# Performance work log

Hardware: AMD Instinct MI355X
Metric: run time of the kernel (lower is better)

## Reference

```python
import jax, jax.numpy as jnp
import numpy as np

B, S, H = 2, 2048, 2048
E, K, HID = 8, 2, 4096          # num_experts, top-k, expert hidden (2*H)
NH, HD = 8, 256                  # attention heads, head_dim
MS, MD = 256, 512                # memory_size, memory_dim
RSTEPS, RD = 3, 512              # reasoning steps, reasoning_dim
SCALE = 16.0                     # sqrt(head_dim)


def setup_inputs() -> dict:
    key = jax.random.key(0)
    ks = iter(jax.random.split(key, 64))
    def w(shape, s=0.02):
        return (jax.random.normal(next(ks), shape, jnp.float32) * s)
    z = lambda *shape: jnp.zeros(shape, jnp.float32)
    inp = {
        'hidden_states': jax.random.normal(next(ks), (B, S, H), jnp.float32),
        'attention_mask': jnp.zeros((B, S), jnp.float32),  # 0 = unmasked (faithful: mask*-1e9 added)
        # MoE
        'gate_w': w((H, E)), 'gate_b': z(E),
        'moe_w1': w((E, H, HID)), 'moe_b1': z(E, HID),
        'moe_w2': w((E, HID, H)), 'moe_b2': z(E, H),
        # memory-augmented attention
        'q_w': w((H, H)), 'q_b': z(H),
        'k_w': w((H, H)), 'k_b': z(H),
        'v_w': w((H, H)), 'v_b': z(H),
        'o_w': w((H, H)), 'o_b': z(H),
        'mem_values': jax.random.normal(next(ks), (MS, MD), jnp.float32),
        'mem_proj_w': w((MD, H)), 'mem_proj_b': z(H),
        'mem_attn_w': w((H, MS)), 'mem_attn_b': z(MS),
        # hierarchical reasoning (stacked over steps)
        'rs_w1': w((RSTEPS, H, RD)), 'rs_b1': z(RSTEPS, RD),
        'rs_w2': w((RSTEPS, RD, H)), 'rs_b2': z(RSTEPS, H),
        'ln_g': jnp.ones((RSTEPS, H), jnp.float32), 'ln_b': z(RSTEPS, H),
        'hg_w1': w((RSTEPS, H, H // 4)), 'hg_b1': z(RSTEPS, H // 4),
        'hg_w2': w((RSTEPS, H // 4, 1)), 'hg_b2': z(RSTEPS, 1),
        'integ_w': w((RSTEPS * H, H)), 'integ_b': z(H),
    }
    return inp


def _layernorm(x, g, b, eps=1e-5):
    m = x.mean(-1, keepdims=True)
    v = ((x - m) ** 2).mean(-1, keepdims=True)
    return (x - m) / jnp.sqrt(v + eps) * g + b


def _forward(hidden_states, attention_mask, gate_w, gate_b, moe_w1, moe_b1, moe_w2, moe_b2,
             q_w, q_b, k_w, k_b, v_w, v_b, o_w, o_b, mem_values, mem_proj_w, mem_proj_b,
             mem_attn_w, mem_attn_b, rs_w1, rs_b1, rs_w2, rs_b2, ln_g, ln_b,
             hg_w1, hg_b1, hg_w2, hg_b2, integ_w, integ_b):
    h = hidden_states
    N = B * S
    # ---- Mixture of Experts (top-k routing, dense combine-weight formulation) ----
    x_flat = h.reshape(N, H)
    gate_probs = jax.nn.softmax(x_flat @ gate_w + gate_b, axis=-1)        # [N,E]
    topk_s, topk_i = jax.lax.top_k(gate_probs, K)                          # [N,K]
    topk_p = jax.nn.softmax(topk_s, axis=-1)                               # renormalize over top-k
    comb = jnp.zeros((N, E), x_flat.dtype).at[jnp.arange(N)[:, None], topk_i].add(topk_p)
    h1 = jax.nn.relu(jnp.einsum('nd,edh->neh', x_flat, moe_w1) + moe_b1)   # [N,E,HID]
    eo = jnp.einsum('neh,ehd->ned', h1, moe_w2) + moe_b2                   # [N,E,H]
    moe_out = jnp.einsum('ned,ne->nd', eo, comb).reshape(B, S, H)
    h = h + 0.5 * moe_out
    # ---- Memory-augmented attention ----
    q = (h @ q_w + q_b).reshape(B, S, NH, HD).transpose(0, 2, 1, 3)
    k = (h @ k_w + k_b).reshape(B, S, NH, HD).transpose(0, 2, 1, 3)
    v = (h @ v_w + v_b).reshape(B, S, NH, HD).transpose(0, 2, 1, 3)
    scores = jnp.einsum('bhqd,bhkd->bhqk', q, k) / SCALE
    scores = scores + attention_mask[:, None, None, :] * (-1e9)
    probs = jax.nn.softmax(scores, axis=-1)
    attn = jnp.einsum('bhqk,bhkd->bhqd', probs, v).transpose(0, 2, 1, 3).reshape(B, S, H)
    mem_p = jax.nn.softmax(h @ mem_attn_w + mem_attn_b, axis=-1)           # [B,S,MS]
    mem_o = (mem_p @ mem_values) @ mem_proj_w + mem_proj_b                 # [B,S,H]
    mem_out = (attn + 0.3 * mem_o) @ o_w + o_b
    h = h + mem_out
    # ---- Hierarchical reasoning ----
    cur = h
    outs = []
    for i in range(RSTEPS):
        so = jax.nn.relu(cur @ rs_w1[i] + rs_b1[i]) @ rs_w2[i] + rs_b2[i]
        so = _layernorm(so, ln_g[i], ln_b[i])
        g = jax.nn.sigmoid(jax.nn.relu(cur @ hg_w1[i] + hg_b1[i]) @ hg_w2[i] + hg_b2[i])  # [B,S,1]
        cur = cur + g * so
        outs.append(cur)
    final = jnp.concatenate(outs, axis=-1) @ integ_w + integ_b
    return h + final


def reference(hidden_states, attention_mask, gate_w, gate_b, moe_w1, moe_b1, moe_w2, moe_b2,
              q_w, q_b, k_w, k_b, v_w, v_b, o_w, o_b, mem_values, mem_proj_w, mem_proj_b,
              mem_attn_w, mem_attn_b, rs_w1, rs_b1, rs_w2, rs_b2, ln_g, ln_b,
              hg_w1, hg_b1, hg_w2, hg_b2, integ_w, integ_b):
    return _forward(hidden_states, attention_mask, gate_w, gate_b, moe_w1, moe_b1, moe_w2, moe_b2,
                    q_w, q_b, k_w, k_b, v_w, v_b, o_w, o_b, mem_values, mem_proj_w, mem_proj_b,
                    mem_attn_w, mem_attn_b, rs_w1, rs_b1, rs_w2, rs_b2, ln_g, ln_b,
                    hg_w1, hg_b1, hg_w2, hg_b2, integ_w, integ_b)
```

## Files before the change

kernel.cpp:

```cpp
#include <hip/hip_runtime.h>
#include <string.h>


typedef __attribute__((ext_vector_type(4))) float f32x4;
typedef __attribute__((ext_vector_type(8))) __bf16 bf16x8;

#define NTOK 4096
#define HDIM 2048
#define AS1 __attribute__((address_space(1)))
#define AS3 __attribute__((address_space(3)))

__device__ __forceinline__ unsigned short f2bf(float f) {
  unsigned u = __float_as_uint(f);
  unsigned r = (u + 0x7fffu + ((u >> 16) & 1u)) >> 16;
  return (unsigned short)r;
}
__device__ __forceinline__ float bf2f(unsigned short u) {
  return __uint_as_float(((unsigned)u) << 16);
}
__device__ __forceinline__ void unpack8(uint4 r, float* v) {
  v[0]=bf2f((unsigned short)(r.x&0xffff)); v[1]=bf2f((unsigned short)(r.x>>16));
  v[2]=bf2f((unsigned short)(r.y&0xffff)); v[3]=bf2f((unsigned short)(r.y>>16));
  v[4]=bf2f((unsigned short)(r.z&0xffff)); v[5]=bf2f((unsigned short)(r.z>>16));
  v[6]=bf2f((unsigned short)(r.w&0xffff)); v[7]=bf2f((unsigned short)(r.w>>16));
}
__device__ __forceinline__ uint4 pack8(const float* v) {
  uint4 r;
  r.x = (unsigned)f2bf(v[0]) | ((unsigned)f2bf(v[1])<<16);
  r.y = (unsigned)f2bf(v[2]) | ((unsigned)f2bf(v[3])<<16);
  r.z = (unsigned)f2bf(v[4]) | ((unsigned)f2bf(v[5])<<16);
  r.w = (unsigned)f2bf(v[6]) | ((unsigned)f2bf(v[7])<<16);
  return r;
}

__global__ void k_tconv(const float* __restrict__ in, unsigned short* __restrict__ out,
                        int R, int C, long inB, long outB) {
  __shared__ float tl[32][33];
  const int z = blockIdx.z;
  const float* ip = in + (long)z * inB;
  unsigned short* op = out + (long)z * outB;
  const int tx = threadIdx.x & 31, ty = threadIdx.x >> 5;
  const int c0 = blockIdx.x * 32, r0 = blockIdx.y * 32;
#pragma unroll
  for (int i = 0; i < 4; i++)
    tl[ty + i*8][tx] = ip[(long)(r0 + ty + i*8) * C + c0 + tx];
  __syncthreads();
#pragma unroll
  for (int i = 0; i < 4; i++)
    op[(long)(c0 + ty + i*8) * R + r0 + tx] = f2bf(tl[tx][ty + i*8]);
}

__global__ void k_cvt(const float* __restrict__ in, unsigned short* __restrict__ out, long n4) {
  long i = (long)blockIdx.x * blockDim.x + threadIdx.x;
  if (i < n4) {
    float4 v = ((const float4*)in)[i];
    float vv[4] = {v.x, v.y, v.z, v.w};
    union { unsigned short u[4]; uint2 d; } p;
#pragma unroll
    for (int j = 0; j < 4; j++) p.u[j] = f2bf(vv[j]);
    ((uint2*)out)[i] = p.d;
  }
}

__global__ void k_tvact(const unsigned short* __restrict__ qkv, unsigned short* __restrict__ vT) {
  __shared__ unsigned short tl[32][33];
  const int z = blockIdx.z, b = z >> 3, hh = z & 7;
  const unsigned short* ip = qkv + (long)b * 2048 * 6144 + 4096 + hh * 256;
  unsigned short* op = vT + (long)z * 256 * 2048;
  const int tx = threadIdx.x & 31, ty = threadIdx.x >> 5;
  const int d0 = blockIdx.x * 32, s0 = blockIdx.y * 32;
#pragma unroll
  for (int i = 0; i < 4; i++)
    tl[ty + i*8][tx] = ip[(long)(s0 + ty + i*8) * 6144 + d0 + tx];
  __syncthreads();
#pragma unroll
  for (int i = 0; i < 4; i++)
    op[(long)(d0 + ty + i*8) * 2048 + s0 + tx] = tl[tx][ty + i*8];
}

__global__ void k_maskvec(const float* __restrict__ m, float* __restrict__ mv) {
  int i = blockIdx.x * 256 + threadIdx.x;
  if (i < 4096) mv[i] = -1e9f * m[i];
}

__global__ void k_zero(int* p) { if (threadIdx.x < 8) p[threadIdx.x] = 0; }

__global__ void k_cat3(const float* __restrict__ a, const float* __restrict__ b,
                       const float* __restrict__ c, float* __restrict__ o) {
  int i = blockIdx.x * 256 + threadIdx.x;
  if (i < 2048) { o[i] = a[i]; o[2048 + i] = b[i]; o[4096 + i] = c[i]; }
}

__global__ void k_cat2x3(const float* __restrict__ a, const float* __restrict__ b,
                         float* __restrict__ o) {
  int i = blockIdx.x * 256 + threadIdx.x;
  if (i < 1536) { int s = i >> 9, c = i & 511; o[s * 1024 + c] = a[i]; o[s * 1024 + 512 + c] = b[i]; }
}

__global__ void k_gate(const float* __restrict__ x, const float* __restrict__ gw,
                       const float* __restrict__ gb, int* __restrict__ meta,
                       int* __restrict__ e0a, int* __restrict__ e1a,
                       float* __restrict__ w0a, float* __restrict__ w1a) {
  const int wv = threadIdx.x >> 6, ln = threadIdx.x & 63;
  const int n = blockIdx.x * 4 + wv;
  const float* xr = x + (long)n * HDIM;
  float s[8] = {0,0,0,0,0,0,0,0};
  for (int k = ln; k < HDIM; k += 64) {
    float xv = xr[k];
    const float* g = gw + (long)k * 8;
#pragma unroll
    for (int e = 0; e < 8; e++) s[e] += xv * g[e];
  }
#pragma unroll
  for (int e = 0; e < 8; e++)
    for (int d = 32; d; d >>= 1) s[e] += __shfl_xor(s[e], d);
  if (ln == 0) {
    float mx = -1e30f;
#pragma unroll
    for (int e = 0; e < 8; e++) { s[e] += gb[e]; mx = fmaxf(mx, s[e]); }
    float p[8], sum = 0.f;
#pragma unroll
    for (int e = 0; e < 8; e++) { p[e] = expf(s[e] - mx); sum += p[e]; }
    float inv = 1.f / sum;
#pragma unroll
    for (int e = 0; e < 8; e++) p[e] *= inv;
    int e0 = 0;
    for (int e = 1; e < 8; e++) if (p[e] > p[e0]) e0 = e;
    int e1 = (e0 == 0) ? 1 : 0;
    for (int e = 0; e < 8; e++) if (e != e0 && p[e] > p[e1]) e1 = e;
    float q = expf(p[e1] - p[e0]);
    float w0 = 1.f / (1.f + q), w1 = q / (1.f + q);
    e0a[n] = e0; e1a[n] = e1; w0a[n] = w0; w1a[n] = w1;
    atomicAdd(&meta[e0], 1); atomicAdd(&meta[e1], 1);
  }
}

__global__ void k_buildmap(int* meta) {
  if (threadIdx.x == 0 && blockIdx.x == 0) {
    int cum = 0, nT = 0;
    for (int e = 0; e < 8; e++) {
      int c = meta[e];
      meta[16 + e] = cum; meta[24 + e] = cum + c; meta[8 + e] = 0;
      int t = (c + 127) >> 7;
      for (int i = 0; i < t; i++) { meta[33 + nT] = e; meta[129 + nT] = cum + i * 128; nT++; }
      cum += c;
    }
    meta[32] = nT;
  }
}

__global__ void k_scatter(int* __restrict__ meta, const int* __restrict__ e0a,
                          const int* __restrict__ e1a, int* __restrict__ s0a,
                          int* __restrict__ s1a, int* __restrict__ srcTok) {
  const int n = blockIdx.x * 256 + threadIdx.x;
  if (n < NTOK) {
    int e0 = e0a[n], e1 = e1a[n];
    int s0 = meta[16 + e0] + atomicAdd(&meta[8 + e0], 1);
    int s1 = meta[16 + e1] + atomicAdd(&meta[8 + e1], 1);
    s0a[n] = s0; s1a[n] = s1; srcTok[s0] = n; srcTok[s1] = n;
  }
}

__global__ void k_gather(const unsigned short* __restrict__ xb, const int* __restrict__ srcTok,
                         unsigned short* __restrict__ xg) {
  const int r = blockIdx.x;
  int n = srcTok[r]; if (n < 0 || n >= NTOK) n = 0;
  ((uint4*)(xg + (long)r * HDIM))[threadIdx.x] =
      ((const uint4*)(xb + (long)n * HDIM))[threadIdx.x];
}

__global__ void k_combine(const float* __restrict__ h, const unsigned short* __restrict__ eo,
                          const int* __restrict__ s0a, const int* __restrict__ s1a,
                          const float* __restrict__ w0a, const float* __restrict__ w1a,
                          float* __restrict__ h2, unsigned short* __restrict__ h2b) {
  const int n = blockIdx.x, c = threadIdx.x * 8;
  const float w0 = w0a[n], w1 = w1a[n];
  uint4 a = *(const uint4*)(eo + (long)s0a[n] * HDIM + c);
  uint4 b = *(const uint4*)(eo + (long)s1a[n] * HDIM + c);
  float va[8], vb[8]; unpack8(a, va); unpack8(b, vb);
  const float* hr = h + (long)n * HDIM + c;
  float o[8];
#pragma unroll
  for (int j = 0; j < 8; j++) o[j] = hr[j] + 0.5f * (w0 * va[j] + w1 * vb[j]);
  float* h2r = h2 + (long)n * HDIM + c;
#pragma unroll
  for (int j = 0; j < 8; j++) h2r[j] = o[j];
  *(uint4*)(h2b + (long)n * HDIM + c) = pack8(o);
}

__global__ void k_softmax2048(unsigned short* __restrict__ p) {
  const long r = blockIdx.x;
  unsigned short* row = p + r * 2048;
  const int t = threadIdx.x, wv = t >> 6, ln = t & 63;
  uint4 raw = ((const uint4*)row)[t];
  float v[8]; unpack8(raw, v);
  float m = v[0];
#pragma unroll
  for (int j = 1; j < 8; j++) m = fmaxf(m, v[j]);
  for (int d = 32; d; d >>= 1) m = fmaxf(m, __shfl_xor(m, d));
  __shared__ float sm[4], ssum[4];
  if (ln == 0) sm[wv] = m;
  __syncthreads();
  m = fmaxf(fmaxf(sm[0], sm[1]), fmaxf(sm[2], sm[3]));
  float s = 0.f;
#pragma unroll
  for (int j = 0; j < 8; j++) { v[j] = expf(v[j] - m); s += v[j]; }
  for (int d = 32; d; d >>= 1) s += __shfl_xor(s, d);
  if (ln == 0) ssum[wv] = s;
  __syncthreads();
  s = ssum[0] + ssum[1] + ssum[2] + ssum[3];
  const float inv = 1.f / s;
#pragma unroll
  for (int j = 0; j < 8; j++) v[j] *= inv;
  ((uint4*)row)[t] = pack8(v);
}

__global__ void k_softmax256(const float* __restrict__ in, unsigned short* __restrict__ out) {
  const int wv = threadIdx.x >> 6, ln = threadIdx.x & 63;
  const long r = (long)blockIdx.x * 4 + wv;
  const float4 v4 = ((const float4*)(in + r * 256))[ln];
  float v[4] = {v4.x, v4.y, v4.z, v4.w};
  float m = fmaxf(fmaxf(v[0], v[1]), fmaxf(v[2], v[3]));
  for (int d = 32; d; d >>= 1) m = fmaxf(m, __shfl_xor(m, d));
  float s = 0.f;
#pragma unroll
  for (int j = 0; j < 4; j++) { v[j] = expf(v[j] - m); s += v[j]; }
  for (int d = 32; d; d >>= 1) s += __shfl_xor(s, d);
  const float inv = 1.f / s;
  union { unsigned short u[4]; uint2 d2; } p;
#pragma unroll
  for (int j = 0; j < 4; j++) p.u[j] = f2bf(v[j] * inv);
  ((uint2*)(out + r * 256))[ln] = p.d2;
}

__global__ void k_gdot(const unsigned short* __restrict__ g1, long ld, const float* __restrict__ w,
                       const float* __restrict__ bb, float* __restrict__ gv) {
  const int wv = threadIdx.x >> 6, ln = threadIdx.x & 63;
  const int n = blockIdx.x * 4 + wv;
  uint4 raw = *(const uint4*)(g1 + (long)n * ld + ln * 8);
  float v[8]; unpack8(raw, v);
  const float4 wa = ((const float4*)w)[ln * 2];
  const float4 wb = ((const float4*)w)[ln * 2 + 1];
  float s = v[0]*wa.x + v[1]*wa.y + v[2]*wa.z + v[3]*wa.w
          + v[4]*wb.x + v[5]*wb.y + v[6]*wb.z + v[7]*wb.w;
  for (int d = 32; d; d >>= 1) s += __shfl_xor(s, d);
  if (ln == 0) gv[n] = 1.f / (1.f + expf(-(s + bb[0])));
}

__global__ void k_lnupdate(const float* __restrict__ so, const float* __restrict__ curIn,
                           const float* __restrict__ gv, const float* __restrict__ lng,
                           const float* __restrict__ lnb, float* __restrict__ curOut,
                           unsigned short* __restrict__ curbOut, unsigned short* __restrict__ outs,
                           int step) {
  const int n = blockIdx.x, t = threadIdx.x, wv = t >> 6, ln = t & 63, c = t * 8;
  const float* row = so + (long)n * 2048 + c;
  float x[8];
#pragma unroll
  for (int j = 0; j < 8; j++) x[j] = row[j];
  float s1 = 0.f, s2 = 0.f;
#pragma unroll
  for (int j = 0; j < 8; j++) { s1 += x[j]; s2 += x[j] * x[j]; }
  for (int d = 32; d; d >>= 1) { s1 += __shfl_xor(s1, d); s2 += __shfl_xor(s2, d); }
  __shared__ float a1[4], a2[4];
  if (ln == 0) { a1[wv] = s1; a2[wv] = s2; }
  __syncthreads();
  s1 = a1[0] + a1[1] + a1[2] + a1[3];
  s2 = a2[0] + a2[1] + a2[2] + a2[3];
  const float mean = s1 * (1.f / 2048.f);
  const float var = s2 * (1.f / 2048.f) - mean * mean;
  const float rstd = rsqrtf(var + 1e-5f);
  const float g = gv[n];
  const float* ci = curIn + (long)n * 2048 + c;
  float o[8];
#pragma unroll
  for (int j = 0; j < 8; j++) {
    float l = (x[j] - mean) * rstd * lng[c + j] + lnb[c + j];
    o[j] = ci[j] + g * l;
  }
  float* co = curOut + (long)n * 2048 + c;
#pragma unroll
  for (int j = 0; j < 8; j++) co[j] = o[j];
  *(uint4*)(curbOut + (long)n * 2048 + c) = pack8(o);
  *(uint4*)(outs + (long)n * 6144 + (long)step * 2048 + c) = pack8(o);
}

struct GArgs {
  const unsigned short* A; long lda, aSO, aSI;
  const unsigned short* Bt; long ldb, bSO, bSI;
  int M, N, K;
  const float* adv; long advSO, advSI;
  float alpha, rscale;
  const float* rF; long ldrF, rfSO, rfSI;
  const unsigned short* rB; long ldrB, rbSO, rbSI;
  float* oF; long ldoF, ofSO, ofSI;
  unsigned short* oB; long ldoB, obSO, obSI;
  const int* meta;
};

template <int MOE, int RELU, int RESID, int OUTF, int OUTB>
__global__ __launch_bounds__(512) void gemm_bt(GArgs g) {
  __shared__ unsigned short lds[2 * 16384];
  const int t = threadIdx.x, wv = t >> 6, ln = t & 63, ln15 = ln & 15;
  const int lr8 = ln >> 3;
  const int lsl = (ln & 7) ^ lr8;
  const int bz = blockIdx.z;
  int row0, rowMax;
  const unsigned short *A, *Bt;
  long advO = 0, rFO = 0, rBO = 0, oFO = 0, oBO = 0;
  if constexpr (MOE) {
    const int ty = blockIdx.y;
    if (ty >= g.meta[32]) return;
    const int e = g.meta[33 + ty];
    row0 = g.meta[129 + ty]; rowMax = g.meta[24 + e];
    A = g.A; Bt = g.Bt + (long)e * g.bSO;
    advO = (long)e * g.advSO;
  } else {
    row0 = blockIdx.y << 7; rowMax = g.M;
    const long bo = (long)(bz >> 3), bi = (long)(bz & 7);
    A = g.A + bo * g.aSO + bi * g.aSI;
    Bt = g.Bt + bo * g.bSO + bi * g.bSI;
    advO = bo * g.advSO + bi * g.advSI;
    rFO = bo * g.rfSO + bi * g.rfSI;
    rBO = bo * g.rbSO + bi * g.rbSI;
    oFO = bo * g.ofSO + bi * g.ofSI;
    oBO = bo * g.obSO + bi * g.obSI;
  }
  const int col0 = blockIdx.x << 7;
  const long lda = g.lda, ldb = g.ldb;
  const int wm = (wv >> 2) << 6;
  const int wc = (wv & 3) << 5;

  auto STAGE = [&](int kt, unsigned base) {
    const long kk = ((long)kt << 6) + (lsl << 3);
#pragma unroll
    for (int l = 0; l < 2; ++l) {
      const int rb = (wv << 4) + (l << 3);
      int gr = row0 + rb + lr8;
      if constexpr (MOE) gr = (gr < rowMax) ? gr : (rowMax - 1);
      __builtin_amdgcn_global_load_lds(
          (const AS1 void*)(A + (long)gr * lda + kk),
          (AS3 void*)(lds + base + (rb << 6)), 16, 0, 0);
    }
#pragma unroll
    for (int l = 0; l < 2; ++l) {
      const int rb = (wv << 4) + (l << 3);
      __builtin_amdgcn_global_load_lds(
          (const AS1 void*)(Bt + (long)(col0 + rb + lr8) * ldb + kk),
          (AS3 void*)(lds + base + 8192 + (rb << 6)), 16, 0, 0);
    }
  };

  const f32x4 fz = {0.f, 0.f, 0.f, 0.f};
  f32x4 acc[4][2];
#pragma unroll
  for (int i = 0; i < 4; i++)
#pragma unroll
    for (int j = 0; j < 2; j++) acc[i][j] = fz;

  const int nt = g.K >> 6;

  STAGE(0, 0);
  asm volatile("s_waitcnt vmcnt(0)" ::: "memory");
  __builtin_amdgcn_s_barrier();

  for (int kt = 0; kt < nt; ++kt) {
    const unsigned aB = (kt & 1) ? 16384u : 0u;
    const unsigned nB = aB ^ 16384u;
    bf16x8 af[2][4], bg[2][2];
#pragma unroll
    for (int ks = 0; ks < 2; ++ks) {
      const int kb = (ks << 2) + (ln >> 4);
#pragma unroll
      for (int i = 0; i < 4; ++i) {
        const int r = wm + (i << 4) + ln15;
        af[ks][i] = *(const bf16x8*)(lds + aB + (r << 6) + ((kb ^ (r & 7)) << 3));
      }
#pragma unroll
      for (int j = 0; j < 2; ++j) {
        const int r = wc + (j << 4) + ln15;
        bg[ks][j] = *(const bf16x8*)(lds + aB + 8192 + (r << 6) + ((kb ^ (r & 7)) << 3));
      }
    }
    __builtin_amdgcn_sched_barrier(0);
    if (kt + 1 < nt) STAGE(kt + 1, nB);
    __builtin_amdgcn_sched_barrier(0);
    __builtin_amdgcn_s_setprio(1);
#pragma unroll
    for (int ks = 0; ks < 2; ++ks)
#pragma unroll
      for (int i = 0; i < 4; ++i)
#pragma unroll
        for (int j = 0; j < 2; ++j)
          acc[i][j] = __builtin_amdgcn_mfma_f32_16x16x32_bf16(af[ks][i], bg[ks][j], acc[i][j], 0, 0, 0);
    __builtin_amdgcn_s_setprio(0);
    asm volatile("s_waitcnt vmcnt(0)" ::: "memory");
    __builtin_amdgcn_s_barrier();
  }

#pragma unroll
  for (int i = 0; i < 4; i++) {
#pragma unroll
    for (int j = 0; j < 2; j++) {
      const int cc = col0 + wc + (j << 4) + ln15;
      const float av = g.adv ? g.adv[advO + cc] : 0.f;
#pragma unroll
      for (int r = 0; r < 4; r++) {
        const int rr = row0 + wm + (i << 4) + ((ln >> 4) << 2) + r;
        if (rr < rowMax) {
          float v = g.alpha * acc[i][j][r] + av;
          if constexpr (RELU) v = fmaxf(v, 0.f);
          if constexpr (RESID == 1) v = g.rF[rFO + (long)rr * g.ldrF + cc] + g.rscale * v;
          if constexpr (RESID == 2) v = bf2f(g.rB[rBO + (long)rr * g.ldrB + cc]) + g.rscale * v;
          if constexpr (OUTF) g.oF[oFO + (long)rr * g.ldoF + cc] = v;
          if constexpr (OUTB) g.oB[oBO + (long)rr * g.ldoB + cc] = f2bf(v);
        }
      }
    }
  }
}

static constexpr size_t O_W1T = 0;
static constexpr size_t O_W2T = O_W1T + (size_t)8 * 4096 * 2048 * 2;
static constexpr size_t O_QT  = O_W2T + (size_t)8 * 4096 * 2048 * 2;
static constexpr size_t O_KT  = O_QT + (size_t)2048 * 2048 * 2;
static constexpr size_t O_VWT = O_KT + (size_t)2048 * 2048 * 2;
static constexpr size_t O_OT  = O_VWT + (size_t)2048 * 2048 * 2;
static constexpr size_t O_MAT = O_OT + (size_t)2048 * 2048 * 2;
static constexpr size_t O_MPT = O_MAT + (size_t)256 * 2048 * 2;
static constexpr size_t O_MVT = O_MPT + (size_t)2048 * 512 * 2;
static constexpr size_t O_RH1 = O_MVT + (size_t)512 * 256 * 2;
static constexpr size_t O_RS2 = O_RH1 + (size_t)3 * 1024 * 2048 * 2;
static constexpr size_t O_IGT = O_RS2 + (size_t)3 * 2048 * 512 * 2;
static constexpr size_t O_META= O_IGT + (size_t)2048 * 6144 * 2;
static constexpr size_t O_E0  = O_META + 4096;
static constexpr size_t O_E1  = O_E0 + 16384;
static constexpr size_t O_W0  = O_E1 + 16384;
static constexpr size_t O_W1  = O_W0 + 16384;
static constexpr size_t O_S0  = O_W1 + 16384;
static constexpr size_t O_S1  = O_S0 + 16384;
static constexpr size_t O_SRC = O_S1 + 16384;
static constexpr size_t O_MSK = O_SRC + 32768;
static constexpr size_t O_GV  = O_MSK + 16384;
static constexpr size_t O_QKVB= O_GV + 16384;
static constexpr size_t O_RHB = O_QKVB + 6144 * 4;
static constexpr size_t O_H2  = O_RHB + 3072 * 4;
static constexpr size_t O_H2B = O_H2 + (size_t)4096 * 2048 * 4;
static constexpr size_t O_H3  = O_H2B + (size_t)4096 * 2048 * 2;
static constexpr size_t O_H3B = O_H3 + (size_t)4096 * 2048 * 4;
static constexpr size_t O_ATT = O_H3B + (size_t)4096 * 2048 * 2;
static constexpr size_t O_AO2 = O_ATT + (size_t)4096 * 2048 * 2;
static constexpr size_t O_MLG = O_AO2 + (size_t)4096 * 2048 * 2;
static constexpr size_t O_MPB = O_MLG + (size_t)4096 * 256 * 4;
static constexpr size_t O_MPV = O_MPB + (size_t)4096 * 256 * 2;
static constexpr size_t O_AR  = O_MPV + (size_t)4096 * 512 * 2;
static constexpr size_t O_XB = O_AR;
static constexpr size_t O_XG = O_XB + (size_t)4096 * 2048 * 2;
static constexpr size_t O_H1 = O_XG + (size_t)8192 * 2048 * 2;
static constexpr size_t O_EO = O_H1 + (size_t)8192 * 4096 * 2;
static constexpr size_t O_QB = O_AR;
static constexpr size_t O_VT = O_QB + (size_t)3 * 4096 * 2048 * 2;
static constexpr size_t O_SC = O_VT + (size_t)4096 * 2048 * 2;
static constexpr size_t O_T1 = O_AR;
static constexpr size_t O_SOB= O_T1 + (size_t)4096 * 1024 * 2;
static constexpr size_t O_CUR= O_SOB + (size_t)4096 * 2048 * 4;
static constexpr size_t O_CRB= O_CUR + (size_t)4096 * 2048 * 4;
static constexpr size_t O_OUS= O_CRB + (size_t)4096 * 2048 * 2;

extern "C" void kernel_launch(void* const* d_in, const int* in_sizes, int n_in,
                              void* d_out, int out_size, void* d_ws, size_t ws_size,
                              hipStream_t stream) {
  (void)in_sizes; (void)n_in; (void)out_size; (void)ws_size;
  const float* h        = (const float*)d_in[0];
  const float* mask     = (const float*)d_in[1];
  const float* gate_w   = (const float*)d_in[2];
  const float* gate_b   = (const float*)d_in[3];
  const float* moe_w1   = (const float*)d_in[4];
  const float* moe_b1   = (const float*)d_in[5];
  const float* moe_w2   = (const float*)d_in[6];
  const float* moe_b2   = (const float*)d_in[7];
  const float* q_w      = (const float*)d_in[8];
  const float* q_b      = (const float*)d_in[9];
  const float* k_w      = (const float*)d_in[10];
  const float* k_b      = (const float*)d_in[11];
  const float* v_w      = (const float*)d_in[12];
  const float* v_b      = (const float*)d_in[13];
  const float* o_w      = (const float*)d_in[14];
  const float* o_b      = (const float*)d_in[15];
  const float* mem_vals = (const float*)d_in[16];
  const float* mproj_w  = (const float*)d_in[17];
  const float* mproj_b  = (const float*)d_in[18];
  const float* mattn_w  = (const float*)d_in[19];
  const float* mattn_b  = (const float*)d_in[20];
  const float* rs_w1    = (const float*)d_in[21];
  const float* rs_b1    = (const float*)d_in[22];
  const float* rs_w2    = (const float*)d_in[23];
  const float* rs_b2    = (const float*)d_in[24];
  const float* ln_g     = (const float*)d_in[25];
  const float* ln_b     = (const float*)d_in[26];
  const float* hg_w1    = (const float*)d_in[27];
  const float* hg_b1    = (const float*)d_in[28];
  const float* hg_w2    = (const float*)d_in[29];
  const float* hg_b2    = (const float*)d_in[30];
  const float* integ_w  = (const float*)d_in[31];
  const float* integ_b  = (const float*)d_in[32];

  char* ws = (char*)d_ws;
  auto U = [&](size_t o) { return (unsigned short*)(ws + o); };
  auto F = [&](size_t o) { return (float*)(ws + o); };
  auto I = [&](size_t o) { return (int*)(ws + o); };

  k_tconv<<<dim3(128, 64, 8), 256, 0, stream>>>(moe_w1, U(O_W1T), 2048, 4096, 8388608, 8388608);
  k_tconv<<<dim3(64, 128, 8), 256, 0, stream>>>(moe_w2, U(O_W2T), 4096, 2048, 8388608, 8388608);
  k_tconv<<<dim3(64, 64, 1), 256, 0, stream>>>(q_w, U(O_QT), 2048, 2048, 0, 0);
  k_tconv<<<dim3(64, 64, 1), 256, 0, stream>>>(k_w, U(O_KT), 2048, 2048, 0, 0);
  k_tconv<<<dim3(64, 64, 1), 256, 0, stream>>>(v_w, U(O_VWT), 2048, 2048, 0, 0);
  k_tconv<<<dim3(64, 64, 1), 256, 0, stream>>>(o_w, U(O_OT), 2048, 2048, 0, 0);
  k_tconv<<<dim3(8, 64, 1), 256, 0, stream>>>(mattn_w, U(O_MAT), 2048, 256, 0, 0);
  k_tconv<<<dim3(64, 16, 1), 256, 0, stream>>>(mproj_w, U(O_MPT), 512, 2048, 0, 0);
  k_tconv<<<dim3(16, 8, 1), 256, 0, stream>>>(mem_vals, U(O_MVT), 256, 512, 0, 0);
  k_tconv<<<dim3(16, 64, 3), 256, 0, stream>>>(rs_w1, U(O_RH1), 2048, 512, 2048 * 512, 1024 * 2048);
  k_tconv<<<dim3(16, 64, 3), 256, 0, stream>>>(hg_w1, U(O_RH1) + (size_t)512 * 2048, 2048, 512,
                                               2048 * 512, 1024 * 2048);
  k_tconv<<<dim3(64, 16, 3), 256, 0, stream>>>(rs_w2, U(O_RS2), 512, 2048, 512 * 2048, 512 * 2048);
  k_tconv<<<dim3(64, 192, 1), 256, 0, stream>>>(integ_w, U(O_IGT), 6144, 2048, 0, 0);
  k_cvt<<<8192, 256, 0, stream>>>(h, U(O_XB), 2097152);
  k_maskvec<<<16, 256, 0, stream>>>(mask, F(O_MSK));
  k_cat3<<<8, 256, 0, stream>>>(q_b, k_b, v_b, F(O_QKVB));
  k_cat2x3<<<6, 256, 0, stream>>>(rs_b1, hg_b1, F(O_RHB));
  k_zero<<<1, 64, 0, stream>>>(I(O_META));

  k_gate<<<1024, 256, 0, stream>>>(h, gate_w, gate_b, I(O_META), I(O_E0), I(O_E1), F(O_W0), F(O_W1));
  k_buildmap<<<1, 1, 0, stream>>>(I(O_META));
  k_scatter<<<16, 256, 0, stream>>>(I(O_META), I(O_E0), I(O_E1), I(O_S0), I(O_S1), I(O_SRC));
  k_gather<<<8192, 256, 0, stream>>>(U(O_XB), I(O_SRC), U(O_XG));

  GArgs z0; memset(&z0, 0, sizeof(z0)); z0.alpha = 1.f; z0.rscale = 1.f;
  {
    GArgs g = z0;
    g.A = U(O_XG); g.lda = 2048;
    g.Bt = U(O_W1T); g.ldb = 2048; g.bSO = (long)4096 * 2048;
    g.N = 4096; g.K = 2048;
    g.adv = moe_b1; g.advSO = 4096;
    g.oB = U(O_H1); g.ldoB = 4096;
    g.meta = I(O_META);
    gemm_bt<1, 1, 0, 0, 1><<<dim3(32, 72, 1), 512, 0, stream>>>(g);
  }
  {
    GArgs g = z0;
    g.A = U(O_H1); g.lda = 4096;
    g.Bt = U(O_W2T); g.ldb = 4096; g.bSO = (long)2048 * 4096;
    g.N = 2048; g.K = 4096;
    g.adv = moe_b2; g.advSO = 2048;
    g.oB = U(O_EO); g.ldoB = 2048;
    g.meta = I(O_META);
    gemm_bt<1, 0, 0, 0, 1><<<dim3(16, 72, 1), 512, 0, stream>>>(g);
  }
  k_combine<<<4096, 256, 0, stream>>>(h, U(O_EO), I(O_S0), I(O_S1), F(O_W0), F(O_W1),
                                      F(O_H2), U(O_H2B));

  {
    GArgs g = z0;
    g.A = U(O_H2B); g.lda = 2048; g.M = 4096; g.N = 6144; g.K = 2048;
    g.Bt = U(O_QT); g.ldb = 2048;
    g.adv = F(O_QKVB);
    g.oB = U(O_QB); g.ldoB = 6144;
    gemm_bt<0, 0, 0, 0, 1><<<dim3(48, 32, 1), 512, 0, stream>>>(g);
  }
  k_tvact<<<dim3(8, 64, 16), 256, 0, stream>>>(U(O_QB), U(O_VT));
  {
    GArgs g = z0;
    g.A = U(O_QB); g.lda = 6144; g.aSO = 12582912; g.aSI = 256;
    g.Bt = U(O_QB) + 2048; g.ldb = 6144; g.bSO = 12582912; g.bSI = 256;
    g.M = 2048; g.N = 2048; g.K = 256;
    g.adv = F(O_MSK); g.advSO = 2048; g.advSI = 0;
    g.alpha = 0.0625f;
    g.oB = U(O_SC); g.ldoB = 2048; g.obSO = 33554432; g.obSI = 4194304;
    gemm_bt<0, 0, 0, 0, 1><<<dim3(16, 16, 16), 512, 0, stream>>>(g);
  }
  k_softmax2048<<<32768, 256, 0, stream>>>(U(O_SC));
  {
    GArgs g = z0;
    g.A = U(O_SC); g.lda = 2048; g.aSO = 33554432; g.aSI = 4194304;
    g.Bt = U(O_VT); g.ldb = 2048; g.bSO = 4194304; g.bSI = 524288;
    g.M = 2048; g.N = 256; g.K = 2048;
    g.oB = U(O_ATT); g.ldoB = 2048; g.obSO = 4194304; g.obSI = 256;
    gemm_bt<0, 0, 0, 0, 1><<<dim3(2, 16, 16), 512, 0, stream>>>(g);
  }
  {
    GArgs g = z0;
    g.A = U(O_H2B); g.lda = 2048; g.Bt = U(O_MAT); g.ldb = 2048;
    g.M = 4096; g.N = 256; g.K = 2048;
    g.adv = mattn_b;
    g.oF = F(O_MLG); g.ldoF = 256;
    gemm_bt<0, 0, 0, 1, 0><<<dim3(2, 32, 1), 512, 0, stream>>>(g);
  }
  k_softmax256<<<1024, 256, 0, stream>>>(F(O_MLG), U(O_MPB));
  {
    GArgs g = z0;
    g.A = U(O_MPB); g.lda = 256; g.Bt = U(O_MVT); g.ldb = 256;
    g.M = 4096; g.N = 512; g.K = 256;
    g.oB = U(O_MPV); g.ldoB = 512;
    gemm_bt<0, 0, 0, 0, 1><<<dim3(4, 32, 1), 512, 0, stream>>>(g);
  }
  {
    GArgs g = z0;
    g.A = U(O_MPV); g.lda = 512; g.Bt = U(O_MPT); g.ldb = 512;
    g.M = 4096; g.N = 2048; g.K = 512;
    g.adv = mproj_b;
    g.rB = U(O_ATT); g.ldrB = 2048; g.rscale = 0.3f;
    g.oB = U(O_AO2); g.ldoB = 2048;
    gemm_bt<0, 0, 2, 0, 1><<<dim3(16, 32, 1), 512, 0, stream>>>(g);
  }
  {
    GArgs g = z0;
    g.A = U(O_AO2); g.lda = 2048; g.Bt = U(O_OT); g.ldb = 2048;
    g.M = 4096; g.N = 2048; g.K = 2048;
    g.adv = o_b;
    g.rF = F(O_H2); g.ldrF = 2048; g.rscale = 1.f;
    g.oF = F(O_H3); g.ldoF = 2048;
    g.oB = U(O_H3B); g.ldoB = 2048;
    gemm_bt<0, 0, 1, 1, 1><<<dim3(16, 32, 1), 512, 0, stream>>>(g);
  }

  for (int i = 0; i < 3; i++) {
    const unsigned short* curb = (i == 0) ? U(O_H3B) : U(O_CRB);
    const float* curf = (i == 0) ? F(O_H3) : F(O_CUR);
    {
      GArgs g = z0;
      g.A = curb; g.lda = 2048;
      g.Bt = U(O_RH1) + (size_t)i * 1024 * 2048; g.ldb = 2048;
      g.M = 4096; g.N = 1024; g.K = 2048;
      g.adv = F(O_RHB) + i * 1024;
      g.oB = U(O_T1); g.ldoB = 1024;
      gemm_bt<0, 1, 0, 0, 1><<<dim3(8, 32, 1), 512, 0, stream>>>(g);
    }
    {
      GArgs g = z0;
      g.A = U(O_T1); g.lda = 1024;
      g.Bt = U(O_RS2) + (size_t)i * 2048 * 512; g.ldb = 512;
      g.M = 4096; g.N = 2048; g.K = 512;
      g.adv = rs_b2 + i * 2048;
      g.oF = F(O_SOB); g.ldoF = 2048;
      gemm_bt<0, 0, 0, 1, 0><<<dim3(16, 32, 1), 512, 0, stream>>>(g);
    }
    k_gdot<<<1024, 256, 0, stream>>>(U(O_T1) + 512, 1024, hg_w2 + i * 512, hg_b2 + i, F(O_GV));
    k_lnupdate<<<4096, 256, 0, stream>>>(F(O_SOB), curf, F(O_GV), ln_g + i * 2048,
                                         ln_b + i * 2048, F(O_CUR), U(O_CRB), U(O_OUS), i);
  }
  {
    GArgs g = z0;
    g.A = U(O_OUS); g.lda = 6144; g.Bt = U(O_IGT); g.ldb = 6144;
    g.M = 4096; g.N = 2048; g.K = 6144;
    g.adv = integ_b;
    g.rF = F(O_H3); g.ldrF = 2048; g.rscale = 1.f;
    g.oF = (float*)d_out; g.ldoF = 2048;
    gemm_bt<0, 0, 1, 1, 0><<<dim3(16, 32, 1), 512, 0, stream>>>(g);
  }
}
```

Measured before the change: 1.738 ms.

## Add 256x256-tile GEMM kernel for MoE, QKV and score GEMMs

Adds a gemm256 kernel with 256x256 output tiles (each wave computes 128x64) and double-buffered 64 KB LDS, and uses it for the two MoE expert GEMMs, the QKV projection and the attention-score GEMM. MoE tile mapping in buildmap switches to 256-row groups to match. Larger tiles raise arithmetic intensity and reuse per LDS load. The loop now interleaves the A-fragment LDS reads with the MFMAs instead of loading all fragments up front. The cost is higher register pressure (128 accumulator floats per lane), one block per CU, and more padded rows wasted in the MoE tiles. The old gemm_bt is kept without the MoE path for the remaining GEMMs.

```diff
diff --git a/kernel.cpp b/kernel.cpp
--- a/kernel.cpp
+++ b/kernel.cpp
@@ -141,8 +141,8 @@
     for (int e = 0; e < 8; e++) {
       int c = meta[e];
       meta[16 + e] = cum; meta[24 + e] = cum + c; meta[8 + e] = 0;
-      int t = (c + 127) >> 7;
-      for (int i = 0; i < t; i++) { meta[33 + nT] = e; meta[129 + nT] = cum + i * 128; nT++; }
+      int t = (c + 255) >> 8;
+      for (int i = 0; i < t; i++) { meta[33 + nT] = e; meta[129 + nT] = cum + i * 256; nT++; }
       cum += c;
     }
     meta[32] = nT;
@@ -300,6 +300,114 @@
 template <int MOE, int RELU, int RESID, int OUTF, int OUTB>
 __global__ __launch_bounds__(512) void gemm_bt(GArgs g) {
   __shared__ unsigned short lds[2 * 16384];
+  const int t = threadIdx.x, wv = t >> 6, ln = t & 63, ln15 = ln & 15;
+  const int lr8 = ln >> 3;
+  const int lsl = (ln & 7) ^ lr8;
+  const int bz = blockIdx.z;
+  int row0, rowMax;
+  const unsigned short *A, *Bt;
+  long advO = 0, rFO = 0, rBO = 0, oFO = 0, oBO = 0;
+  {
+    row0 = blockIdx.y << 7; rowMax = g.M;
+    const long bo = (long)(bz >> 3), bi = (long)(bz & 7);
+    A = g.A + bo * g.aSO + bi * g.aSI;
+    Bt = g.Bt + bo * g.bSO + bi * g.bSI;
+    advO = bo * g.advSO + bi * g.advSI;
+    rFO = bo * g.rfSO + bi * g.rfSI;
+    rBO = bo * g.rbSO + bi * g.rbSI;
+    oFO = bo * g.ofSO + bi * g.ofSI;
+    oBO = bo * g.obSO + bi * g.obSI;
+  }
+  const int col0 = blockIdx.x << 7;
+  const long lda = g.lda, ldb = g.ldb;
+  const int wm = (wv >> 2) << 6;
+  const int wc = (wv & 3) << 5;
+
+  auto STAGE = [&](int kt, unsigned base) {
+    const long kk = ((long)kt << 6) + (lsl << 3);
+#pragma unroll
+    for (int l = 0; l < 2; ++l) {
+      const int rb = (wv << 4) + (l << 3);
+      int gr = row0 + rb + lr8;
+      __builtin_amdgcn_global_load_lds(
+          (const AS1 void*)(A + (long)gr * lda + kk),
+          (AS3 void*)(lds + base + (rb << 6)), 16, 0, 0);
+    }
+#pragma unroll
+    for (int l = 0; l < 2; ++l) {
+      const int rb = (wv << 4) + (l << 3);
+      __builtin_amdgcn_global_load_lds(
+          (const AS1 void*)(Bt + (long)(col0 + rb + lr8) * ldb + kk),
+          (AS3 void*)(lds + base + 8192 + (rb << 6)), 16, 0, 0);
+    }
+  };
+
+  const f32x4 fz = {0.f, 0.f, 0.f, 0.f};
+  f32x4 acc[4][2];
+#pragma unroll
+  for (int i = 0; i < 4; i++)
+#pragma unroll
+    for (int j = 0; j < 2; j++) acc[i][j] = fz;
+
+  const int nt = g.K >> 6;
+
+  STAGE(0, 0);
+  asm volatile("s_waitcnt vmcnt(0)" ::: "memory");
+  __builtin_amdgcn_s_barrier();
+
+  for (int kt = 0; kt < nt; ++kt) {
+    const unsigned aB = (kt & 1) ? 16384u : 0u;
+    const unsigned nB = aB ^ 16384u;
+    if (kt + 1 < nt) STAGE(kt + 1, nB);
+#pragma unroll
+    for (int ks = 0; ks < 2; ++ks) {
+      const int kb = (ks << 2) + (ln >> 4);
+      bf16x8 bg[2];
+#pragma unroll
+      for (int j = 0; j < 2; ++j) {
+        const int r = wc + (j << 4) + ln15;
+        bg[j] = *(const bf16x8*)(lds + aB + 8192 + (r << 6) + ((kb ^ (r & 7)) << 3));
+      }
+      __builtin_amdgcn_s_setprio(1);
+#pragma unroll
+      for (int i = 0; i < 4; ++i) {
+        const int r = wm + (i << 4) + ln15;
+        bf16x8 a = *(const bf16x8*)(lds + aB + (r << 6) + ((kb ^ (r & 7)) << 3));
+#pragma unroll
+        for (int j = 0; j < 2; ++j)
+          acc[i][j] = __builtin_amdgcn_mfma_f32_16x16x32_bf16(a, bg[j], acc[i][j], 0, 0, 0);
+      }
+      __builtin_amdgcn_s_setprio(0);
+    }
+    asm volatile("s_waitcnt vmcnt(0)" ::: "memory");
+    __builtin_amdgcn_s_barrier();
+  }
+
+#pragma unroll
+  for (int i = 0; i < 4; i++) {
+#pragma unroll
+    for (int j = 0; j < 2; j++) {
+      const int cc = col0 + wc + (j << 4) + ln15;
+      const float av = g.adv ? g.adv[advO + cc] : 0.f;
+#pragma unroll
+      for (int r = 0; r < 4; r++) {
+        const int rr = row0 + wm + (i << 4) + ((ln >> 4) << 2) + r;
+        if (rr < rowMax) {
+          float v = g.alpha * acc[i][j][r] + av;
+          if constexpr (RELU) v = fmaxf(v, 0.f);
+          if constexpr (RESID == 1) v = g.rF[rFO + (long)rr * g.ldrF + cc] + g.rscale * v;
+          if constexpr (RESID == 2) v = bf2f(g.rB[rBO + (long)rr * g.ldrB + cc]) + g.rscale * v;
+          if constexpr (OUTF) g.oF[oFO + (long)rr * g.ldoF + cc] = v;
+          if constexpr (OUTB) g.oB[oBO + (long)rr * g.ldoB + cc] = f2bf(v);
+        }
+      }
+    }
+  }
+}
+
+template <int MOE, int RELU, int RESID, int OUTF, int OUTB>
+__global__ __launch_bounds__(512, 1) void gemm256(GArgs g) {
+  __shared__ unsigned short lds[2 * 32768];
   const int t = threadIdx.x, wv = t >> 6, ln = t & 63, ln15 = ln & 15;
   const int lr8 = ln >> 3;
   const int lsl = (ln & 7) ^ lr8;
@@ -315,7 +423,7 @@
     A = g.A; Bt = g.Bt + (long)e * g.bSO;
     advO = (long)e * g.advSO;
   } else {
-    row0 = blockIdx.y << 7; rowMax = g.M;
+    row0 = blockIdx.y << 8; rowMax = g.M;
     const long bo = (long)(bz >> 3), bi = (long)(bz & 7);
     A = g.A + bo * g.aSO + bi * g.aSI;
     Bt = g.Bt + bo * g.bSO + bi * g.bSI;
@@ -325,16 +433,16 @@
     oFO = bo * g.ofSO + bi * g.ofSI;
     oBO = bo * g.obSO + bi * g.obSI;
   }
-  const int col0 = blockIdx.x << 7;
+  const int col0 = blockIdx.x << 8;
   const long lda = g.lda, ldb = g.ldb;
-  const int wm = (wv >> 2) << 6;
-  const int wc = (wv & 3) << 5;
+  const int wm = (wv >> 2) << 7;
+  const int wn = (wv & 3) << 6;
 
   auto STAGE = [&](int kt, unsigned base) {
     const long kk = ((long)kt << 6) + (lsl << 3);
 #pragma unroll
-    for (int l = 0; l < 2; ++l) {
-      const int rb = (wv << 4) + (l << 3);
+    for (int l = 0; l < 4; ++l) {
+      const int rb = ((l << 3) + wv) << 3;
       int gr = row0 + rb + lr8;
       if constexpr (MOE) gr = (gr < rowMax) ? gr : (rowMax - 1);
       __builtin_amdgcn_global_load_lds(
@@ -342,20 +450,20 @@
           (AS3 void*)(lds + base + (rb << 6)), 16, 0, 0);
     }
 #pragma unroll
-    for (int l = 0; l < 2; ++l) {
-      const int rb = (wv << 4) + (l << 3);
+    for (int l = 0; l < 4; ++l) {
+      const int rb = ((l << 3) + wv) << 3;
       __builtin_amdgcn_global_load_lds(
           (const AS1 void*)(Bt + (long)(col0 + rb + lr8) * ldb + kk),
-          (AS3 void*)(lds + base + 8192 + (rb << 6)), 16, 0, 0);
+          (AS3 void*)(lds + base + 16384 + (rb << 6)), 16, 0, 0);
     }
   };
 
   const f32x4 fz = {0.f, 0.f, 0.f, 0.f};
-  f32x4 acc[4][2];
-#pragma unroll
-  for (int i = 0; i < 4; i++)
-#pragma unroll
-    for (int j = 0; j < 2; j++) acc[i][j] = fz;
+  f32x4 acc[8][4];
+#pragma unroll
+  for (int i = 0; i < 8; i++)
+#pragma unroll
+    for (int j = 0; j < 4; j++) acc[i][j] = fz;
 
   const int nt = g.K >> 6;
 
@@ -364,44 +472,38 @@
   __builtin_amdgcn_s_barrier();
 
   for (int kt = 0; kt < nt; ++kt) {
-    const unsigned aB = (kt & 1) ? 16384u : 0u;
-    const unsigned nB = aB ^ 16384u;
-    bf16x8 af[2][4], bg[2][2];
+    const unsigned aB = (kt & 1) ? 32768u : 0u;
+    const unsigned nB = aB ^ 32768u;
+    if (kt + 1 < nt) STAGE(kt + 1, nB);
 #pragma unroll
     for (int ks = 0; ks < 2; ++ks) {
       const int kb = (ks << 2) + (ln >> 4);
-#pragma unroll
-      for (int i = 0; i < 4; ++i) {
+      bf16x8 bg[4];
+#pragma unroll
+      for (int j = 0; j < 4; ++j) {
+        const int r = wn + (j << 4) + ln15;
+        bg[j] = *(const bf16x8*)(lds + aB + 16384 + (r << 6) + ((kb ^ (r & 7)) << 3));
+      }
+      __builtin_amdgcn_s_setprio(1);
+#pragma unroll
+      for (int i = 0; i < 8; ++i) {
         const int r = wm + (i << 4) + ln15;
-        af[ks][i] = *(const bf16x8*)(lds + aB + (r << 6) + ((kb ^ (r & 7)) << 3));
+        bf16x8 a = *(const bf16x8*)(lds + aB + (r << 6) + ((kb ^ (r & 7)) << 3));
+#pragma unroll
+        for (int j = 0; j < 4; ++j)
+          acc[i][j] = __builtin_amdgcn_mfma_f32_16x16x32_bf16(a, bg[j], acc[i][j], 0, 0, 0);
       }
-#pragma unroll
-      for (int j = 0; j < 2; ++j) {
-        const int r = wc + (j << 4) + ln15;
-        bg[ks][j] = *(const bf16x8*)(lds + aB + 8192 + (r << 6) + ((kb ^ (r & 7)) << 3));
-      }
-    }
-    __builtin_amdgcn_sched_barrier(0);
-    if (kt + 1 < nt) STAGE(kt + 1, nB);
-    __builtin_amdgcn_sched_barrier(0);
-    __builtin_amdgcn_s_setprio(1);
-#pragma unroll
-    for (int ks = 0; ks < 2; ++ks)
-#pragma unroll
-      for (int i = 0; i < 4; ++i)
-#pragma unroll
-        for (int j = 0; j < 2; ++j)
-          acc[i][j] = __builtin_amdgcn_mfma_f32_16x16x32_bf16(af[ks][i], bg[ks][j], acc[i][j], 0, 0, 0);
-    __builtin_amdgcn_s_setprio(0);
+      __builtin_amdgcn_s_setprio(0);
+    }
     asm volatile("s_waitcnt vmcnt(0)" ::: "memory");
     __builtin_amdgcn_s_barrier();
   }
 
 #pragma unroll
-  for (int i = 0; i < 4; i++) {
-#pragma unroll
-    for (int j = 0; j < 2; j++) {
-      const int cc = col0 + wc + (j << 4) + ln15;
+  for (int i = 0; i < 8; i++) {
+#pragma unroll
+    for (int j = 0; j < 4; j++) {
+      const int cc = col0 + wn + (j << 4) + ln15;
       const float av = g.adv ? g.adv[advO + cc] : 0.f;
 #pragma unroll
       for (int r = 0; r < 4; r++) {
@@ -543,7 +645,7 @@
     g.adv = moe_b1; g.advSO = 4096;
     g.oB = U(O_H1); g.ldoB = 4096;
     g.meta = I(O_META);
-    gemm_bt<1, 1, 0, 0, 1><<<dim3(32, 72, 1), 512, 0, stream>>>(g);
+    gemm256<1, 1, 0, 0, 1><<<dim3(16, 40, 1), 512, 0, stream>>>(g);
   }
   {
     GArgs g = z0;
@@ -553,7 +655,7 @@
     g.adv = moe_b2; g.advSO = 2048;
     g.oB = U(O_EO); g.ldoB = 2048;
     g.meta = I(O_META);
-    gemm_bt<1, 0, 0, 0, 1><<<dim3(16, 72, 1), 512, 0, stream>>>(g);
+    gemm256<1, 0, 0, 0, 1><<<dim3(8, 40, 1), 512, 0, stream>>>(g);
   }
   k_combine<<<4096, 256, 0, stream>>>(h, U(O_EO), I(O_S0), I(O_S1), F(O_W0), F(O_W1),
                                       F(O_H2), U(O_H2B));
@@ -564,7 +666,7 @@
     g.Bt = U(O_QT); g.ldb = 2048;
     g.adv = F(O_QKVB);
     g.oB = U(O_QB); g.ldoB = 6144;
-    gemm_bt<0, 0, 0, 0, 1><<<dim3(48, 32, 1), 512, 0, stream>>>(g);
+    gemm256<0, 0, 0, 0, 1><<<dim3(24, 16, 1), 512, 0, stream>>>(g);
   }
   k_tvact<<<dim3(8, 64, 16), 256, 0, stream>>>(U(O_QB), U(O_VT));
   {
@@ -575,7 +677,7 @@
     g.adv = F(O_MSK); g.advSO = 2048; g.advSI = 0;
     g.alpha = 0.0625f;
     g.oB = U(O_SC); g.ldoB = 2048; g.obSO = 33554432; g.obSI = 4194304;
-    gemm_bt<0, 0, 0, 0, 1><<<dim3(16, 16, 16), 512, 0, stream>>>(g);
+    gemm256<0, 0, 0, 0, 1><<<dim3(8, 8, 16), 512, 0, stream>>>(g);
   }
   k_softmax2048<<<32768, 256, 0, stream>>>(U(O_SC));
   {
```

Measured after the change: 1.872 ms. 1.08x slower.
